# Kernel optimization log

Hardware: AMD Instinct MI355X
Metric: run time of the kernel (lower is better)

Reference implementation:

```python
import jax, jax.numpy as jnp
import numpy as np

B, L, H, R = 8, 128, 768, 24


def setup_inputs() -> dict:
    key = jax.random.key(0)
    ks = jax.random.split(key, 12)
    s = 0.02  # init scale
    f32 = jnp.float32
    inp = {
        "embed_tokens": jax.random.normal(ks[0], (B, L, H), f32),
        "attention_mask": jnp.ones((B, L), f32),
        "target_rel": jax.random.randint(ks[1], (B,), 0, R),
        # relation-judgement head
        "W_hr": jax.random.normal(ks[2], (H, H // 2), f32) * s,
        "b_hr": jnp.zeros((H // 2,), f32),
        "W_rj": jax.random.normal(ks[3], (H // 2, R), f32) * s,
        "b_rj": jnp.zeros((R,), f32),
        # relation embedding
        "rel_emb": jax.random.normal(ks[4], (R, H), f32) * s,
        # correspondence matrix head (input is concat -> 2H)
        "W_corr": jax.random.normal(ks[5], (2 * H, H), f32) * s,
        "b_corr": jnp.zeros((H,), f32),
        "W_gc": jax.random.normal(ks[6], (H, 1), f32) * s,
        "b_gc": jnp.zeros((1,), f32),
        # subject tagging head (fusion_type='concat' -> 2H in, H hidden)
        "W_sh": jax.random.normal(ks[7], (2 * H, H), f32) * s,
        "b_sh": jnp.zeros((H,), f32),
        "W_st": jax.random.normal(ks[8], (H, 3), f32) * s,
        "b_st": jnp.zeros((3,), f32),
        # object tagging head
        "W_oh": jax.random.normal(ks[9], (2 * H, H), f32) * s,
        "b_oh": jnp.zeros((H,), f32),
        "W_ot": jax.random.normal(ks[10], (H, 3), f32) * s,
        "b_ot": jnp.zeros((3,), f32),
    }
    return inp


def reference(embed_tokens, attention_mask, target_rel,
              W_hr, b_hr, W_rj, b_rj, rel_emb,
              W_corr, b_corr, W_gc, b_gc,
              W_sh, b_sh, W_st, b_st,
              W_oh, b_oh, W_ot, b_ot):
    # ---- stage 1: masked mean-pool + relation judgement (dropout = identity at inference)
    masked = embed_tokens * attention_mask[:, :, None]            # [B,L,H]
    pool = jnp.sum(masked, axis=1) / jnp.sum(attention_mask, axis=1)[:, None]  # [B,H]
    rel_hidden = jax.nn.relu(pool @ W_hr + b_hr)                  # [B,H/2]
    stage1 = rel_hidden @ W_rj + b_rj                             # [B,R]

    # ---- correspondence matrix: concat[b,i,j] = [embed[b,j], embed[b,i]]
    # Decompose concat-linear: concat @ W_corr = embed_j @ W1 + embed_i @ W2
    W1, W2 = W_corr[:H_dim(embed_tokens)], W_corr[H_dim(embed_tokens):]
    A = embed_tokens @ W1                                         # [B,L,H] (j-index part)
    C = embed_tokens @ W2                                         # [B,L,H] (i-index part)
    corres_hidden = jax.nn.relu(A[:, None, :, :] + C[:, :, None, :] + b_corr)  # [B,L,L,H]
    pred_corres = corres_hidden @ W_gc + b_gc                     # [B,L,L,1]

    # ---- relation-fused tagging (mode == 'train')
    re = rel_emb[target_rel]                                      # [B,H]
    Bsz, Lsz, Hsz = embed_tokens.shape
    fusion = jnp.concatenate(
        [jnp.broadcast_to(re[:, None, :], (Bsz, Lsz, Hsz)), embed_tokens], axis=-1)  # [B,L,2H]
    subj = jax.nn.relu(fusion @ W_sh + b_sh) @ W_st + b_st        # [B,L,3]
    obj = jax.nn.relu(fusion @ W_oh + b_oh) @ W_ot + b_ot         # [B,L,3]

    return stage1, subj, obj, pred_corres


def H_dim(x):
    return x.shape[-1]
```

## Files before the change

### kernel.cpp

```cpp
#include <hip/hip_runtime.h>
#include <hip/hip_bf16.h>

#define BD   8
#define LD   128
#define HD   768
#define RD   24
#define H2D  384
#define NF   1536
#define WSZ  589824

typedef __attribute__((ext_vector_type(8))) short bf16x8;
typedef __attribute__((ext_vector_type(4))) float f32x4;
typedef _Float16 f16x2 __attribute__((ext_vector_type(2)));

__device__ __forceinline__ short f2bf(float f) {
    __hip_bfloat16 h = __float2bfloat16(f);
    return *reinterpret_cast<short*>(&h);
}

__device__ __forceinline__ unsigned int packh2(float a, float b) {
    f16x2 p;
    p[0] = (_Float16)a;
    p[1] = (_Float16)b;
    return __builtin_bit_cast(unsigned int, p);
}

__device__ __forceinline__ void dstep(float& acc, unsigned int cu, f16x2 a, f16x2 w) {
    f16x2 t = a + __builtin_bit_cast(f16x2, cu);
    f16x2 z = {(_Float16)0.f, (_Float16)0.f};
    t = __builtin_elementwise_max(t, z);
#if __has_builtin(__builtin_amdgcn_fdot2)
    acc = __builtin_amdgcn_fdot2(t, w, acc, false);
#else
    acc += (float)t[0] * (float)w[0] + (float)t[1] * (float)w[1];
#endif
}

__global__ __launch_bounds__(256) void prep_kernel(
        const float* __restrict__ embed, const float* __restrict__ mask,
        const float* __restrict__ rel_emb, const int* __restrict__ trel,
        const float* __restrict__ W_corr,
        const float* __restrict__ W_sh, const float* __restrict__ b_sh,
        const float* __restrict__ W_oh, const float* __restrict__ b_oh,
        const float* __restrict__ b_st, const float* __restrict__ b_ot,
        const float* __restrict__ W_gc,
        float* __restrict__ pool, float* __restrict__ biasrel,
        unsigned short* __restrict__ embedB, unsigned short* __restrict__ WT,
        unsigned int* __restrict__ wg16,
        float* __restrict__ out_subj, float* __restrict__ out_obj) {
    const int q = blockIdx.x, tid = threadIdx.x;

    if (q < 96) {
        const int b = q / 12, c = q % 12;
        __shared__ float mrow[LD];
        __shared__ float msum;
        __shared__ float part[4][64];
        if (tid < LD) mrow[tid] = mask[b * LD + tid];
        __syncthreads();
        if (tid == 0) {
            float s = 0.f;
            for (int l = 0; l < LD; ++l) s += mrow[l];
            msum = s;
        }
        __syncthreads();
        const int lc = tid >> 6, hh = tid & 63;
        const int h = c * 64 + hh;
        float acc = 0.f;
        const float* base = embed + ((size_t)b * LD + lc * 32) * HD + h;
#pragma unroll 8
        for (int i = 0; i < 32; ++i) acc += base[(size_t)i * HD] * mrow[lc * 32 + i];
        part[lc][hh] = acc;
        __syncthreads();
        if (lc == 0)
            pool[b * HD + h] = (part[0][hh] + part[1][hh] + part[2][hh] + part[3][hh]) / msum;
    } else if (q < 120) {
        const int c = q - 96;
        __shared__ float reAll[8][HD];
        __shared__ float part[4][8][64];
        for (int u = tid; u < 8 * HD; u += 256) {
            const int b = u / HD, k = u - b * HD;
            reAll[b][k] = rel_emb[(size_t)trel[b] * HD + k];
        }
        if (c == 0) {
            for (int u = tid; u < 3 * LD * BD; u += 256) {
                const int b = u / (3 * LD), rem = u - b * (3 * LD);
                const int l = rem / 3, t = rem - 3 * l;
                out_subj[(b * LD + l) * 3 + t] = b_st[t];
                out_obj [(b * LD + l) * 3 + t] = b_ot[t];
            }
        }
        __syncthreads();
        const int kc = tid >> 6, nn = tid & 63;
        const int n = c * 64 + nn;
        const float* Wp; int col;
        if (n < HD) { Wp = W_sh; col = n; }
        else        { Wp = W_oh; col = n - HD; }
        float acc[8] = {};
        for (int i = 0; i < 192; ++i) {
            const int k = kc * 192 + i;
            const float w = Wp[(size_t)k * HD + col];
#pragma unroll
            for (int b = 0; b < 8; ++b) acc[b] += reAll[b][k] * w;
        }
#pragma unroll
        for (int b = 0; b < 8; ++b) part[kc][b][nn] = acc[b];
        __syncthreads();
        {
            const float bb = (n < HD) ? b_sh[col] : b_oh[col];
            const int b0 = kc, b1 = kc + 4;
            float s0 = part[0][b0][nn] + part[1][b0][nn] + part[2][b0][nn] + part[3][b0][nn];
            float s1 = part[0][b1][nn] + part[1][b1][nn] + part[2][b1][nn] + part[3][b1][nn];
            biasrel[b0 * NF + n] = s0 + bb;
            biasrel[b1 * NF + n] = s1 + bb;
        }
    } else if (q < 216) {
        const int base = (q - 120) * 8192;
#pragma unroll
        for (int it = 0; it < 4; ++it) {
            const int off = base + it * 2048 + tid * 8;
            float4 v0 = *(const float4*)&embed[off];
            float4 v1 = *(const float4*)&embed[off + 4];
            bf16x8 p;
            p[0] = f2bf(v0.x); p[1] = f2bf(v0.y); p[2] = f2bf(v0.z); p[3] = f2bf(v0.w);
            p[4] = f2bf(v1.x); p[5] = f2bf(v1.y); p[6] = f2bf(v1.z); p[7] = f2bf(v1.w);
            *(bf16x8*)&embedB[off] = p;
        }
    } else if (q < 792) {
        const int qq = q - 216;
        const int w = qq / 144, t = qq % 144;
        const int kt = t / 12, nt = t % 12;
        const float* src = (w == 0) ? W_corr
                         : (w == 1) ? W_corr + WSZ
                         : (w == 2) ? W_sh + WSZ
                                    : W_oh + WSZ;
        unsigned short* dst = WT + (size_t)w * WSZ;
        __shared__ float tile[64 * 65];
        const int r = tid >> 2, c4 = (tid & 3) * 16;
#pragma unroll
        for (int i = 0; i < 4; ++i) {
            float4 v = *(const float4*)&src[(size_t)(kt * 64 + r) * HD + nt * 64 + c4 + i * 4];
            tile[r * 65 + c4 + i * 4 + 0] = v.x;
            tile[r * 65 + c4 + i * 4 + 1] = v.y;
            tile[r * 65 + c4 + i * 4 + 2] = v.z;
            tile[r * 65 + c4 + i * 4 + 3] = v.w;
        }
        __syncthreads();
        bf16x8 p0, p1;
#pragma unroll
        for (int j = 0; j < 8; ++j) {
            p0[j] = f2bf(tile[(c4 + j) * 65 + r]);
            p1[j] = f2bf(tile[(c4 + 8 + j) * 65 + r]);
        }
        unsigned short* o = dst + (size_t)(nt * 64 + r) * HD + kt * 64 + c4;
        *(bf16x8*)(o)     = p0;
        *(bf16x8*)(o + 8) = p1;
    } else {
        for (int u = tid; u < 384; u += 256) {
            const int n = (u & 15) + (u >> 4) * 32;
            wg16[u] = packh2(W_gc[n], W_gc[n + 16]);
        }
    }
}

__global__ __launch_bounds__(256) void biggemm(
        const unsigned short* __restrict__ embedB,
        const unsigned short* __restrict__ WT,
        const float* __restrict__ biasrel,
        const float* __restrict__ W_st, const float* __restrict__ W_ot,
        const float* __restrict__ pool,
        const float* __restrict__ W_hr, const float* __restrict__ b_hr,
        const float* __restrict__ b_corr,
        unsigned int* __restrict__ AC16, float* __restrict__ out_subj,
        float* __restrict__ out_obj, float* __restrict__ rh) {
    const int tid = threadIdx.x;

    if (blockIdx.x >= 24) {
        const int b = blockIdx.y >> 1;
        const int c = (blockIdx.x - 24) * 2 + (blockIdx.y & 1);
        __shared__ float prow[HD];
        __shared__ float rpart[4][64];
        for (int k = tid; k < HD; k += 256) prow[k] = pool[b * HD + k];
        __syncthreads();
        const int kc = tid >> 6, nn = tid & 63;
        const int n = c * 64 + nn;
        float acc = 0.f;
#pragma unroll 8
        for (int i = 0; i < 192; ++i) {
            const int k = kc * 192 + i;
            acc += prow[k] * W_hr[(size_t)k * H2D + n];
        }
        rpart[kc][nn] = acc;
        __syncthreads();
        if (kc == 0)
            rh[b * H2D + n] = fmaxf(rpart[0][nn] + rpart[1][nn] + rpart[2][nn] + rpart[3][nn] + b_hr[n], 0.f);
        return;
    }

    __shared__ __align__(16) short As [64][76];
    __shared__ __align__(16) short Bs0[64][76];
    __shared__ __align__(16) short Bs1[64][76];
    __shared__ float partial[64][3];

    const int bn0 = blockIdx.x * 64;
    const int bm0 = blockIdx.y * 64;

    const unsigned short* W0 = (bn0 < HD) ? WT : WT + WSZ;
    const unsigned short* W1 = (bn0 < HD) ? WT + 2 * (size_t)WSZ : WT + 3 * (size_t)WSZ;
    const int col0 = (bn0 < HD) ? bn0 : bn0 - HD;

    if (tid < 192) partial[tid / 3][tid % 3] = 0.f;

    const int row = tid >> 2;
    const int kc8 = (tid & 3) * 8;
    const size_t eaBase = (size_t)(bm0 + row) * HD + kc8;
    const size_t waBase = (size_t)(col0 + row) * HD + kc8;

    const int lane = tid & 63;
    const int wv = tid >> 6;
    const int wm = (wv >> 1) * 32;
    const int wn = (wv & 1) * 32;
    const int fr = lane & 15;
    const int kq = (lane >> 4) * 8;
    const int mq = (lane >> 4) * 4;

    f32x4 c00 = {0.f,0.f,0.f,0.f}, c01 = c00, c10 = c00, c11 = c00;
    f32x4 h00 = c00, h01 = c00, h10 = c00, h11 = c00;

    bf16x8 av0, av1, b0v0, b0v1, b1v0, b1v1;
    {
        av0  = *(const bf16x8*)&embedB[eaBase];
        av1  = *(const bf16x8*)&embedB[eaBase + 32];
        b0v0 = *(const bf16x8*)&W0[waBase];
        b0v1 = *(const bf16x8*)&W0[waBase + 32];
        b1v0 = *(const bf16x8*)&W1[waBase];
        b1v1 = *(const bf16x8*)&W1[waBase + 32];
    }

    for (int kt = 0; kt < 12; ++kt) {
        __syncthreads();
        *(bf16x8*)&As [row][kc8]      = av0;
        *(bf16x8*)&As [row][kc8 + 32] = av1;
        *(bf16x8*)&Bs0[row][kc8]      = b0v0;
        *(bf16x8*)&Bs0[row][kc8 + 32] = b0v1;
        *(bf16x8*)&Bs1[row][kc8]      = b1v0;
        *(bf16x8*)&Bs1[row][kc8 + 32] = b1v1;
        __syncthreads();

        if (kt < 11) {
            const int k0 = (kt + 1) << 6;
            av0  = *(const bf16x8*)&embedB[eaBase + k0];
            av1  = *(const bf16x8*)&embedB[eaBase + k0 + 32];
            b0v0 = *(const bf16x8*)&W0[waBase + k0];
            b0v1 = *(const bf16x8*)&W0[waBase + k0 + 32];
            b1v0 = *(const bf16x8*)&W1[waBase + k0];
            b1v1 = *(const bf16x8*)&W1[waBase + k0 + 32];
        }

#pragma unroll
        for (int kk = 0; kk < 2; ++kk) {
            const int kx = kq + kk * 32;
            bf16x8 a0 = *(bf16x8*)&As[wm + fr][kx];
            bf16x8 a1 = *(bf16x8*)&As[wm + 16 + fr][kx];
            bf16x8 b0 = *(bf16x8*)&Bs0[wn + fr][kx];
            bf16x8 b1 = *(bf16x8*)&Bs0[wn + 16 + fr][kx];
            bf16x8 d0 = *(bf16x8*)&Bs1[wn + fr][kx];
            bf16x8 d1 = *(bf16x8*)&Bs1[wn + 16 + fr][kx];
            c00 = __builtin_amdgcn_mfma_f32_16x16x32_bf16(a0, b0, c00, 0, 0, 0);
            c01 = __builtin_amdgcn_mfma_f32_16x16x32_bf16(a0, b1, c01, 0, 0, 0);
            c10 = __builtin_amdgcn_mfma_f32_16x16x32_bf16(a1, b0, c10, 0, 0, 0);
            c11 = __builtin_amdgcn_mfma_f32_16x16x32_bf16(a1, b1, c11, 0, 0, 0);
            h00 = __builtin_amdgcn_mfma_f32_16x16x32_bf16(a0, d0, h00, 0, 0, 0);
            h01 = __builtin_amdgcn_mfma_f32_16x16x32_bf16(a0, d1, h01, 0, 0, 0);
            h10 = __builtin_amdgcn_mfma_f32_16x16x32_bf16(a1, d0, h10, 0, 0, 0);
            h11 = __builtin_amdgcn_mfma_f32_16x16x32_bf16(a1, d1, h11, 0, 0, 0);
        }
    }

    {
        const int dbase = ((bn0 + wn) >> 5) << 4;
        float bc0 = 0.f, bc1 = 0.f;
        if (bn0 >= HD) {
            bc0 = b_corr[bn0 + wn + fr - HD];
            bc1 = b_corr[bn0 + wn + fr - HD + 16];
        }
#pragma unroll
        for (int i = 0; i < 2; ++i) {
            f32x4 a0 = (i == 0) ? c00 : c10;
            f32x4 a1 = (i == 0) ? c01 : c11;
#pragma unroll
            for (int r = 0; r < 4; ++r) {
                const int mrow = bm0 + wm + i * 16 + mq + r;
                AC16[(size_t)mrow * 768 + dbase + fr] = packh2(a0[r] + bc0, a1[r] + bc1);
            }
        }
    }

    {
        const float* brl = biasrel + (size_t)(bm0 / LD) * NF;
        const float* Wt = (bn0 < HD) ? W_st : W_ot;
        float* op = (bn0 < HD) ? out_subj : out_obj;
        float pt[8][3] = {};
#pragma unroll
        for (int j = 0; j < 2; ++j) {
            const int ncol = bn0 + wn + j * 16 + fr;
            const int ncl = (bn0 < HD) ? ncol : ncol - HD;
            const float wt0 = Wt[ncl * 3 + 0];
            const float wt1 = Wt[ncl * 3 + 1];
            const float wt2 = Wt[ncl * 3 + 2];
            const float bias = brl[ncol];
#pragma unroll
            for (int i = 0; i < 2; ++i) {
                f32x4 a = (i == 0) ? (j == 0 ? h00 : h01) : (j == 0 ? h10 : h11);
#pragma unroll
                for (int r = 0; r < 4; ++r) {
                    const float v = fmaxf(a[r] + bias, 0.f);
                    pt[i * 4 + r][0] += v * wt0;
                    pt[i * 4 + r][1] += v * wt1;
                    pt[i * 4 + r][2] += v * wt2;
                }
            }
        }
#pragma unroll
        for (int mask = 1; mask < 16; mask <<= 1) {
#pragma unroll
            for (int x = 0; x < 8; ++x)
#pragma unroll
                for (int t = 0; t < 3; ++t)
                    pt[x][t] += __shfl_xor(pt[x][t], mask, 64);
        }
        if (fr == 0) {
#pragma unroll
            for (int i = 0; i < 2; ++i)
#pragma unroll
                for (int r = 0; r < 4; ++r)
#pragma unroll
                    for (int t = 0; t < 3; ++t)
                        atomicAdd(&partial[wm + i * 16 + mq + r][t], pt[i * 4 + r][t]);
        }
        __syncthreads();
        if (tid < 192) {
            const int m = tid / 3, t = tid % 3;
            atomicAdd(&op[(size_t)(bm0 + m) * 3 + t], partial[m][t]);
        }
    }
}

__global__ __launch_bounds__(512) void corres_kernel(
        const unsigned int* __restrict__ AC16,
        const unsigned int* __restrict__ wg16,
        const float* __restrict__ b_gc,
        const float* __restrict__ rh,
        const float* __restrict__ W_rj, const float* __restrict__ b_rj,
        float* __restrict__ out, float* __restrict__ out_stage1) {
    const int b = blockIdx.y;
    const int tid = threadIdx.x;

    if (blockIdx.x == 32) {
        __shared__ float rl[H2D];
        __shared__ float spart[8][RD];
        if (tid < H2D) rl[tid] = rh[b * H2D + tid];
        __syncthreads();
        if (tid < 8 * RD) {
            const int n = tid % RD, kc = tid / RD;
            float acc = 0.f;
#pragma unroll 8
            for (int i = 0; i < 48; ++i) {
                const int k = kc * 48 + i;
                acc += rl[k] * W_rj[k * RD + n];
            }
            spart[kc][n] = acc;
        }
        __syncthreads();
        if (tid < RD) {
            float s = b_rj[tid];
#pragma unroll
            for (int q = 0; q < 8; ++q) s += spart[q][tid];
            out_stage1[b * RD + tid] = s;
        }
        return;
    }

    const int xt = blockIdx.x >> 1;
    const int yg = blockIdx.x & 1;
    const int X0 = xt * 8, Y0 = yg * 64;
    const int lane = tid & 63;
    const int w8 = tid >> 6;

    __shared__ float lds_out[8][64];
    lds_out[w8][lane] = 0.f;

    f16x2 av[48], wv[48];
    {
        const uint4* ap = (const uint4*)(AC16 + ((size_t)(b * LD + Y0 + lane)) * 768 + w8 * 48);
        const uint4* wp = (const uint4*)(wg16 + w8 * 48);
#pragma unroll
        for (int k = 0; k < 12; ++k) {
            const uint4 va = ap[k];
            const uint4 vw = wp[k];
            av[4*k+0] = __builtin_bit_cast(f16x2, va.x);
            av[4*k+1] = __builtin_bit_cast(f16x2, va.y);
            av[4*k+2] = __builtin_bit_cast(f16x2, va.z);
            av[4*k+3] = __builtin_bit_cast(f16x2, va.w);
            wv[4*k+0] = __builtin_bit_cast(f16x2, vw.x);
            wv[4*k+1] = __builtin_bit_cast(f16x2, vw.y);
            wv[4*k+2] = __builtin_bit_cast(f16x2, vw.z);
            wv[4*k+3] = __builtin_bit_cast(f16x2, vw.w);
        }
    }
    __syncthreads();

    float acc[8];
#pragma unroll
    for (int x = 0; x < 8; ++x) acc[x] = 0.f;

    const uint4* cbase = (const uint4*)(AC16 + ((size_t)(b * LD + X0)) * 768 + 384 + w8 * 48);
    uint4 cc[12];
#pragma unroll
    for (int k = 0; k < 12; ++k) cc[k] = cbase[k];

#pragma unroll
    for (int x = 0; x < 8; ++x) {
        uint4 nn[12];
        if (x < 7) {
            const uint4* np = cbase + (size_t)(x + 1) * 192;
#pragma unroll
            for (int k = 0; k < 12; ++k) nn[k] = np[k];
        }
        float a = acc[x];
#pragma unroll
        for (int k = 0; k < 12; ++k) {
            dstep(a, cc[k].x, av[4*k+0], wv[4*k+0]);
            dstep(a, cc[k].y, av[4*k+1], wv[4*k+1]);
            dstep(a, cc[k].z, av[4*k+2], wv[4*k+2]);
            dstep(a, cc[k].w, av[4*k+3], wv[4*k+3]);
        }
        acc[x] = a;
        if (x < 7) {
#pragma unroll
            for (int k = 0; k < 12; ++k) cc[k] = nn[k];
        }
    }

#pragma unroll
    for (int x = 0; x < 8; ++x) atomicAdd(&lds_out[x][lane], acc[x]);
    __syncthreads();
    {
        const int xo = tid >> 6, yo = tid & 63;
        out[((size_t)(b * LD + X0 + xo)) * LD + Y0 + yo] = lds_out[xo][yo] + b_gc[0];
    }
}

extern "C" void kernel_launch(void* const* d_in, const int* in_sizes, int n_in,
                              void* d_out, int out_size, void* d_ws, size_t ws_size,
                              hipStream_t stream) {
    const float* embed   = (const float*)d_in[0];
    const float* mask    = (const float*)d_in[1];
    const int*   trel    = (const int*)d_in[2];
    const float* W_hr    = (const float*)d_in[3];
    const float* b_hr    = (const float*)d_in[4];
    const float* W_rj    = (const float*)d_in[5];
    const float* b_rj    = (const float*)d_in[6];
    const float* rel_emb = (const float*)d_in[7];
    const float* W_corr  = (const float*)d_in[8];
    const float* b_corr  = (const float*)d_in[9];
    const float* W_gc    = (const float*)d_in[10];
    const float* b_gc    = (const float*)d_in[11];
    const float* W_sh    = (const float*)d_in[12];
    const float* b_sh    = (const float*)d_in[13];
    const float* W_st    = (const float*)d_in[14];
    const float* b_st    = (const float*)d_in[15];
    const float* W_oh    = (const float*)d_in[16];
    const float* b_oh    = (const float*)d_in[17];
    const float* W_ot    = (const float*)d_in[18];
    const float* b_ot    = (const float*)d_in[19];
    float* out = (float*)d_out;

    float* ws = (float*)d_ws;
    unsigned int* AC16 = (unsigned int*)ws;
    float* biasrel = ws + 786432;
    float* rh      = ws + 786432 + 12288;
    float* pool    = ws + 786432 + 12288 + 3072;
    unsigned int* wg16 = (unsigned int*)(ws + 807936);
    unsigned short* embedB = (unsigned short*)(ws + 808320);
    unsigned short* WT     = (unsigned short*)(ws + 808320 + 393216);

    float* out_stage1 = out;
    float* out_subj   = out + 192;
    float* out_obj    = out + 3264;
    float* out_corr   = out + 6336;

    prep_kernel<<<793, 256, 0, stream>>>(embed, mask, rel_emb, trel, W_corr,
                                         W_sh, b_sh, W_oh, b_oh, b_st, b_ot, W_gc,
                                         pool, biasrel, embedB, WT, wg16,
                                         out_subj, out_obj);

    biggemm<<<dim3(27, 16), 256, 0, stream>>>(embedB, WT, biasrel, W_st, W_ot,
                                              pool, W_hr, b_hr, b_corr,
                                              AC16, out_subj, out_obj, rh);

    corres_kernel<<<dim3(33, BD), 512, 0, stream>>>(AC16, wg16, b_gc,
                                                    rh, W_rj, b_rj, out_corr, out_stage1);
}
```

Measured before the change: 153.8 us.

## Stream GEMM tiles directly to LDS with double-buffered swizzled layout

Replaces the register-staged global-to-LDS copy in the projection GEMM with direct global_load_lds transfers into a double-buffered, XOR-swizzled shared-memory tile. The next K-tile now loads while the current one is computed, with one barrier per iteration instead of two. The swizzle replaces row padding to avoid LDS bank conflicts. This adds reliance on manual waitcnt and raw barriers for correctness and doubles the LDS footprint, which could lower occupancy.

```diff
diff --git a/kernel.cpp b/kernel.cpp
--- a/kernel.cpp
+++ b/kernel.cpp
@@ -34,6 +34,20 @@
 #else
     acc += (float)t[0] * (float)w[0] + (float)t[1] * (float)w[1];
 #endif
+}
+
+typedef const __attribute__((address_space(1))) unsigned int* as1_u32p;
+typedef __attribute__((address_space(3))) unsigned int* as3_u32p;
+__device__ __forceinline__ void gload16(const void* g, void* l) {
+    __builtin_amdgcn_global_load_lds((as1_u32p)g, (as3_u32p)l, 16, 0, 0);
+}
+
+__device__ __forceinline__ void block_sync() {
+    asm volatile("" ::: "memory");
+    __builtin_amdgcn_sched_barrier(0);
+    __builtin_amdgcn_s_barrier();
+    __builtin_amdgcn_sched_barrier(0);
+    asm volatile("" ::: "memory");
 }
 
 __global__ __launch_bounds__(256) void prep_kernel(
@@ -196,9 +210,7 @@
         return;
     }
 
-    __shared__ __align__(16) short As [64][76];
-    __shared__ __align__(16) short Bs0[64][76];
-    __shared__ __align__(16) short Bs1[64][76];
+    __shared__ __align__(16) short ldsb[2][3][64][64];
     __shared__ float partial[64][3];
 
     const int bn0 = blockIdx.x * 64;
@@ -209,62 +221,45 @@
     const int col0 = (bn0 < HD) ? bn0 : bn0 - HD;
 
     if (tid < 192) partial[tid / 3][tid % 3] = 0.f;
-
-    const int row = tid >> 2;
-    const int kc8 = (tid & 3) * 8;
-    const size_t eaBase = (size_t)(bm0 + row) * HD + kc8;
-    const size_t waBase = (size_t)(col0 + row) * HD + kc8;
 
     const int lane = tid & 63;
     const int wv = tid >> 6;
     const int wm = (wv >> 1) * 32;
     const int wn = (wv & 1) * 32;
     const int fr = lane & 15;
-    const int kq = (lane >> 4) * 8;
     const int mq = (lane >> 4) * 4;
+
+    const int g8  = lane >> 3;
+    const int xsw = ((lane & 7) ^ g8) << 3;
+    const int sw = (fr & 7) << 4;
 
     f32x4 c00 = {0.f,0.f,0.f,0.f}, c01 = c00, c10 = c00, c11 = c00;
     f32x4 h00 = c00, h01 = c00, h10 = c00, h11 = c00;
 
-    bf16x8 av0, av1, b0v0, b0v1, b1v0, b1v1;
-    {
-        av0  = *(const bf16x8*)&embedB[eaBase];
-        av1  = *(const bf16x8*)&embedB[eaBase + 32];
-        b0v0 = *(const bf16x8*)&W0[waBase];
-        b0v1 = *(const bf16x8*)&W0[waBase + 32];
-        b1v0 = *(const bf16x8*)&W1[waBase];
-        b1v1 = *(const bf16x8*)&W1[waBase + 32];
-    }
-
-    for (int kt = 0; kt < 12; ++kt) {
-        __syncthreads();
-        *(bf16x8*)&As [row][kc8]      = av0;
-        *(bf16x8*)&As [row][kc8 + 32] = av1;
-        *(bf16x8*)&Bs0[row][kc8]      = b0v0;
-        *(bf16x8*)&Bs0[row][kc8 + 32] = b0v1;
-        *(bf16x8*)&Bs1[row][kc8]      = b1v0;
-        *(bf16x8*)&Bs1[row][kc8 + 32] = b1v1;
-        __syncthreads();
-
-        if (kt < 11) {
-            const int k0 = (kt + 1) << 6;
-            av0  = *(const bf16x8*)&embedB[eaBase + k0];
-            av1  = *(const bf16x8*)&embedB[eaBase + k0 + 32];
-            b0v0 = *(const bf16x8*)&W0[waBase + k0];
-            b0v1 = *(const bf16x8*)&W0[waBase + k0 + 32];
-            b1v0 = *(const bf16x8*)&W1[waBase + k0];
-            b1v1 = *(const bf16x8*)&W1[waBase + k0 + 32];
-        }
-
+    auto stage = [&](int kt, int bsel) {
+#pragma unroll
+        for (int j = 0; j < 2; ++j) {
+            const int seg = wv * 2 + j;
+            const size_t gofs = (size_t)(seg * 8 + g8) * HD + (kt << 6) + xsw;
+            gload16(embedB + (size_t)bm0 * HD + gofs, &ldsb[bsel][0][seg * 8][0]);
+            gload16(W0 + (size_t)col0 * HD + gofs,    &ldsb[bsel][1][seg * 8][0]);
+            gload16(W1 + (size_t)col0 * HD + gofs,    &ldsb[bsel][2][seg * 8][0]);
+        }
+    };
+
+    auto compute = [&](int bsel) {
+        const char* base0 = (const char*)&ldsb[bsel][0][0][0];
+        const char* base1 = (const char*)&ldsb[bsel][1][0][0];
+        const char* base2 = (const char*)&ldsb[bsel][2][0][0];
 #pragma unroll
         for (int kk = 0; kk < 2; ++kk) {
-            const int kx = kq + kk * 32;
-            bf16x8 a0 = *(bf16x8*)&As[wm + fr][kx];
-            bf16x8 a1 = *(bf16x8*)&As[wm + 16 + fr][kx];
-            bf16x8 b0 = *(bf16x8*)&Bs0[wn + fr][kx];
-            bf16x8 b1 = *(bf16x8*)&Bs0[wn + 16 + fr][kx];
-            bf16x8 d0 = *(bf16x8*)&Bs1[wn + fr][kx];
-            bf16x8 d1 = *(bf16x8*)&Bs1[wn + 16 + fr][kx];
+            const int kx2 = (((lane >> 4) * 16 + kk * 64)) ^ sw;
+            bf16x8 a0 = *(const bf16x8*)(base0 + (wm + fr) * 128 + kx2);
+            bf16x8 a1 = *(const bf16x8*)(base0 + (wm + 16 + fr) * 128 + kx2);
+            bf16x8 b0 = *(const bf16x8*)(base1 + (wn + fr) * 128 + kx2);
+            bf16x8 b1 = *(const bf16x8*)(base1 + (wn + 16 + fr) * 128 + kx2);
+            bf16x8 d0 = *(const bf16x8*)(base2 + (wn + fr) * 128 + kx2);
+            bf16x8 d1 = *(const bf16x8*)(base2 + (wn + 16 + fr) * 128 + kx2);
             c00 = __builtin_amdgcn_mfma_f32_16x16x32_bf16(a0, b0, c00, 0, 0, 0);
             c01 = __builtin_amdgcn_mfma_f32_16x16x32_bf16(a0, b1, c01, 0, 0, 0);
             c10 = __builtin_amdgcn_mfma_f32_16x16x32_bf16(a1, b0, c10, 0, 0, 0);
@@ -274,7 +269,21 @@
             h10 = __builtin_amdgcn_mfma_f32_16x16x32_bf16(a1, d0, h10, 0, 0, 0);
             h11 = __builtin_amdgcn_mfma_f32_16x16x32_bf16(a1, d1, h11, 0, 0, 0);
         }
-    }
+    };
+
+    stage(0, 0);
+    asm volatile("s_waitcnt vmcnt(0)" ::: "memory");
+    block_sync();
+
+    int cur = 0;
+    for (int kt = 0; kt < 11; ++kt) {
+        stage(kt + 1, cur ^ 1);
+        compute(cur);
+        asm volatile("s_waitcnt vmcnt(0)" ::: "memory");
+        block_sync();
+        cur ^= 1;
+    }
+    compute(cur);
 
     {
         const int dbase = ((bn0 + wn) >> 5) << 4;
@@ -328,6 +337,7 @@
                 for (int t = 0; t < 3; ++t)
                     pt[x][t] += __shfl_xor(pt[x][t], mask, 64);
         }
+        __syncthreads();
         if (fr == 0) {
 #pragma unroll
             for (int i = 0; i < 2; ++i)
```

Result: no change. 152.9 us (-0.6%).
